# Optimization experiments

Measured on AMD Instinct MI355X. Metric: run time of the kernel, lower is better.

## Reference

```python
import math
import jax, jax.numpy as jnp
import numpy as np

B = 2
TMAX = 1024
D = 1024
H = 16
DK = D // H
F = 4096
L = 2
CHUNK = 128
LEFT = 128
RIGHT = 32
EPS = 1e-5


def _build_mask(t_max, chunk, left, right):
    """Replicates EmformerEncoder.create_mask with audio_lens == t_max.
    Returns bool [T, T] where True = masked (disallowed), T = total_right + t_max."""
    num_chunks = math.ceil(t_max / chunk)
    ub = (num_chunks - 1) * right
    body = np.zeros((t_max, t_max), np.float32)
    mleft = np.zeros((t_max, ub), np.float32)
    mdiag = np.zeros((ub, ub), np.float32)
    mright = np.zeros((ub, t_max), np.float32)
    right_indexes = []
    for i in range(num_chunks):
        left_off = max(chunk * i - left, 0)
        start = chunk * i
        end = min(chunk * (i + 1), t_max)
        body[start:end, left_off:end] = 1
        if i == num_chunks - 1:
            break
        rem = t_max - (end + right)
        trl = right if rem >= 0 else t_max - end
        ri = len(right_indexes)
        mleft[start:start + chunk, ri:ri + trl] = 1
        mdiag[ri:ri + trl, ri:ri + trl] = 1
        mright[ri:ri + trl, left_off:end] = 1
        right_indexes += list(range(end, end + trl))
    rs = len(right_indexes)
    mleft = mleft[:, :rs]
    mdiag = mdiag[:rs, :rs]
    mright = mright[:rs, :]
    top = np.concatenate([mdiag, mright], axis=-1)
    bot = np.concatenate([mleft, body], axis=-1)
    m = np.concatenate([top, bot], axis=0)
    return m == 0  # True where attention is NOT allowed


def setup_inputs() -> dict:
    key = jax.random.key(0)
    ks = jax.random.split(key, 8)
    mask2d = _build_mask(TMAX, CHUNK, LEFT, RIGHT)  # [T, T]
    T = mask2d.shape[0]  # 1248
    w = lambda k, shape: jax.random.normal(k, shape, jnp.float32) * 0.02
    inp = {
        "input": jax.random.normal(ks[0], (B, T, D), jnp.float32),
        "ln_in_scale": jnp.ones((L, D), jnp.float32),
        "ln_in_bias": jnp.zeros((L, D), jnp.float32),
        "Wq": w(ks[1], (L, D, D)), "bq": jnp.zeros((L, D), jnp.float32),
        "Wk": w(ks[2], (L, D, D)), "bk": jnp.zeros((L, D), jnp.float32),
        "Wv": w(ks[3], (L, D, D)), "bv": jnp.zeros((L, D), jnp.float32),
        "ln1_scale": jnp.ones((L, D), jnp.float32),
        "ln1_bias": jnp.zeros((L, D), jnp.float32),
        "W1": w(ks[4], (L, D, F)), "b1": jnp.zeros((L, F), jnp.float32),
        "W2": w(ks[5], (L, F, D)), "b2": jnp.zeros((L, D), jnp.float32),
        "ln2_scale": jnp.ones((L, D), jnp.float32),
        "ln2_bias": jnp.zeros((L, D), jnp.float32),
        "mask": jnp.asarray(np.broadcast_to(mask2d[None, None], (B, 1, T, T)).copy()),
    }
    return inp


def _ln(x, scale, bias):
    m = jnp.mean(x, axis=-1, keepdims=True)
    v = jnp.mean(jnp.square(x - m), axis=-1, keepdims=True)
    return (x - m) * jax.lax.rsqrt(v + EPS) * scale + bias


def reference(input, ln_in_scale, ln_in_bias, Wq, bq, Wk, bk, Wv, bv,
              ln1_scale, ln1_bias, W1, b1, W2, b2, ln2_scale, ln2_bias, mask):
    x = input
    Bx, T, _ = x.shape
    scale = 1.0 / math.sqrt(DK)
    for l in range(L):
        h = _ln(x, ln_in_scale[l], ln_in_bias[l])  # pre-LN input (also residual base)
        q = (h @ Wq[l] + bq[l]).reshape(Bx, T, H, DK)
        k = (h @ Wk[l] + bk[l]).reshape(Bx, T, H, DK)
        v = (h @ Wv[l] + bv[l]).reshape(Bx, T, H, DK)
        scores = jnp.einsum('bqhd,bkhd->bhqk', q, k) * scale  # [B,H,T,T]
        scores = jnp.where(mask, -jnp.inf, scores)
        probs = jax.nn.softmax(scores, axis=-1)
        probs = jnp.where(mask, 0.0, probs)  # dropout_attn=0 -> identity
        o = jnp.einsum('bhqk,bkhd->bqhd', probs, v).reshape(Bx, T, D)
        attn_out = o + h
        y = _ln(attn_out, ln1_scale[l], ln1_bias[l])
        y = y @ W1[l] + b1[l]          # note: no activation in original code
        y = y @ W2[l] + b2[l] + attn_out
        x = _ln(y, ln2_scale[l], ln2_bias[l])
    return x
```

## Files before the change

### kernel.cpp

```cpp
#include <hip/hip_runtime.h>
#include <stdint.h>

typedef __attribute__((ext_vector_type(8))) short short8;
typedef __attribute__((ext_vector_type(4))) float f32x4;
typedef __attribute__((ext_vector_type(2))) _Float16 half2_t;

#define DEV __device__ __forceinline__

DEV float bits2f(uint32_t u){ union{uint32_t u;float f;}v; v.u=u; return v.f; }
DEV float bf_lo(uint32_t w){ return bits2f(w<<16); }
DEV float bf_hi(uint32_t w){ return bits2f(w & 0xffff0000u); }
DEV float bf1(uint16_t s){ return bits2f(((uint32_t)s)<<16); }
DEV uint16_t f2bf(float f){ union{float f;uint32_t u;}v; v.f=f; uint32_t u=v.u;
  return (uint16_t)((u + 0x7fffu + ((u>>16)&1u))>>16); }
DEV uint32_t pk16(float a, float b){ union{_Float16 h[2]; uint32_t u;}v;
  v.h[0]=(_Float16)a; v.h[1]=(_Float16)b; return v.u; }
DEV uint16_t f2h(float a){ union{_Float16 h; uint16_t u;}v; v.h=(_Float16)a; return v.u; }
DEV float h2f(uint16_t s){ union{uint16_t u; _Float16 h;}v; v.u=s; return (float)v.h; }

DEV float ldval(const float* p, size_t i){ return p[i]; }
DEV float ldval(const uint16_t* p, size_t i){ return bf1(p[i]); }
DEV void stval(float* p, size_t i, float v){ p[i]=v; }
DEV void stval(uint16_t* p, size_t i, float v){ p[i]=f2bf(v); }

DEV void async16(const void* g, void* l){
#if __has_builtin(__builtin_amdgcn_global_load_lds)
  __builtin_amdgcn_global_load_lds((const __attribute__((address_space(1))) void*)g,
                                   (__attribute__((address_space(3))) void*)l, 16, 0, 0);
#else
  int lane = threadIdx.x & 63;
  *(uint4*)((char*)l + lane*16) = *(const uint4*)((const char*)g);
#endif
}

template<int TM, bool SPLIT>
__global__ __launch_bounds__(256) void gemm_t(
    const uint16_t* __restrict__ A, const uint16_t* __restrict__ Bt,
    const float* __restrict__ bias, void* __restrict__ Cout,
    int N, int K, int kchunk) {
  __shared__ uint16_t sA[TM*32];
  __shared__ uint16_t sB[128*32];
  const int m0 = blockIdx.y*TM, n0 = blockIdx.x*128;
  const int kb = SPLIT ? blockIdx.z*kchunk : 0;
  const int kend = SPLIT ? kb + kchunk : K;
  const int tid = threadIdx.x, wid = tid>>6, lane = tid&63;
  constexpr int WM = TM/2;
  constexpr int MT = WM/16;
  const int wm = (wid&1)*WM, wn = (wid>>1)*64;
  f32x4 acc[MT][4];
  #pragma unroll
  for (int a=0;a<MT;a++)
    #pragma unroll
    for (int b=0;b<4;b++) acc[a][b] = (f32x4){0.f,0.f,0.f,0.f};
  const int lrow = lane>>2, lcol = (lane&3)*8;

  for (int k0 = kb; k0 < kend; k0 += 32) {
    __syncthreads();
    #pragma unroll
    for (int j = 0; j < TM/64; ++j) {
      int r0 = wid*(TM/4) + j*16;
      async16(A + (size_t)(m0 + r0 + lrow)*K + k0 + lcol, &sA[r0*32]);
    }
    #pragma unroll
    for (int j = 0; j < 2; ++j) {
      int r0 = wid*32 + j*16;
      async16(Bt + (size_t)(n0 + r0 + lrow)*K + k0 + lcol, &sB[r0*32]);
    }
    __syncthreads();
    short8 af[MT], bfv[4];
    #pragma unroll
    for (int t=0;t<MT;t++) af[t] = *(const short8*)&sA[(wm + t*16 + (lane&15))*32 + (lane>>4)*8];
    #pragma unroll
    for (int t=0;t<4;t++)  bfv[t] = *(const short8*)&sB[(wn + t*16 + (lane&15))*32 + (lane>>4)*8];
    #pragma unroll
    for (int mt=0;mt<MT;mt++)
      #pragma unroll
      for (int nt=0;nt<4;nt++)
        acc[mt][nt] = __builtin_amdgcn_mfma_f32_16x16x32_bf16(af[mt], bfv[nt], acc[mt][nt], 0,0,0);
  }
  const int cl = lane&15, rl = (lane>>4)*4;
  if (SPLIT) {
    float* Pz = (float*)Cout + (size_t)blockIdx.z*2560*N;
    #pragma unroll
    for (int nt=0;nt<4;nt++) {
      int n = n0 + wn + nt*16 + cl;
      #pragma unroll
      for (int mt=0;mt<MT;mt++)
        #pragma unroll
        for (int r=0;r<4;r++)
          Pz[(size_t)(m0 + wm + mt*16 + rl + r)*N + n] = acc[mt][nt][r];
    }
  } else {
    uint16_t* C = (uint16_t*)Cout;
    #pragma unroll
    for (int nt=0;nt<4;nt++) {
      int n = n0 + wn + nt*16 + cl;
      float bv = bias ? bias[n] : 0.f;
      #pragma unroll
      for (int mt=0;mt<MT;mt++)
        #pragma unroll
        for (int r=0;r<4;r++)
          C[(size_t)(m0 + wm + mt*16 + rl + r)*N + n] = f2bf(acc[mt][nt][r] + bv);
    }
  }
}

template<typename TI, typename TO>
__global__ __launch_bounds__(256) void ln_k(const TI* __restrict__ x,
    const float* __restrict__ sc, const float* __restrict__ bi,
    TO* __restrict__ out) {
  const int row = blockIdx.x, tid = threadIdx.x;
  const size_t base = (size_t)row*1024 + tid*4;
  float v0=ldval(x,base), v1=ldval(x,base+1), v2=ldval(x,base+2), v3=ldval(x,base+3);
  float s = v0+v1+v2+v3;
  float sq = v0*v0+v1*v1+v2*v2+v3*v3;
  #pragma unroll
  for (int off=32; off; off>>=1){ s += __shfl_xor(s,off); sq += __shfl_xor(sq,off); }
  __shared__ float red[8];
  int wid=tid>>6, lane=tid&63;
  if (lane==0){ red[wid]=s; red[4+wid]=sq; }
  __syncthreads();
  s = red[0]+red[1]+red[2]+red[3]; sq = red[4]+red[5]+red[6]+red[7];
  float mean = s*(1.f/1024.f);
  float inv  = rsqrtf(sq*(1.f/1024.f) - mean*mean + 1e-5f);
  int c = tid*4;
  stval(out, base,   (v0-mean)*inv*sc[c]   + bi[c]);
  stval(out, base+1, (v1-mean)*inv*sc[c+1] + bi[c+1]);
  stval(out, base+2, (v2-mean)*inv*sc[c+2] + bi[c+2]);
  stval(out, base+3, (v3-mean)*inv*sc[c+3] + bi[c+3]);
}

template<typename TO>
__global__ __launch_bounds__(256) void ln2_fused(const float* __restrict__ P,
    const float* __restrict__ b2, const uint16_t* __restrict__ resid,
    const float* __restrict__ sc, const float* __restrict__ bi,
    TO* __restrict__ out) {
  const int row = blockIdx.x, tid = threadIdx.x;
  const size_t base = (size_t)row*1024 + tid*4;
  float4 p0 = *(const float4*)(P + base);
  float4 p1 = *(const float4*)(P + (size_t)2560*1024 + base);
  int c = tid*4;
  float v0 = p0.x+p1.x+b2[c]  +bf1(resid[base]);
  float v1 = p0.y+p1.y+b2[c+1]+bf1(resid[base+1]);
  float v2 = p0.z+p1.z+b2[c+2]+bf1(resid[base+2]);
  float v3 = p0.w+p1.w+b2[c+3]+bf1(resid[base+3]);
  float s = v0+v1+v2+v3;
  float sq = v0*v0+v1*v1+v2*v2+v3*v3;
  #pragma unroll
  for (int off=32; off; off>>=1){ s += __shfl_xor(s,off); sq += __shfl_xor(sq,off); }
  __shared__ float red[8];
  int wid=tid>>6, lane=tid&63;
  if (lane==0){ red[wid]=s; red[4+wid]=sq; }
  __syncthreads();
  s = red[0]+red[1]+red[2]+red[3]; sq = red[4]+red[5]+red[6]+red[7];
  float mean = s*(1.f/1024.f);
  float inv  = rsqrtf(sq*(1.f/1024.f) - mean*mean + 1e-5f);
  stval(out, base,   (v0-mean)*inv*sc[c]   + bi[c]);
  stval(out, base+1, (v1-mean)*inv*sc[c+1] + bi[c+1]);
  stval(out, base+2, (v2-mean)*inv*sc[c+2] + bi[c+2]);
  stval(out, base+3, (v3-mean)*inv*sc[c+3] + bi[c+3]);
}

__global__ __launch_bounds__(256) void attn_fused(
    const uint32_t* __restrict__ qkv32, const uint16_t* __restrict__ hres,
    uint16_t* __restrict__ attn_out) {
  const int blk = blockIdx.x;
  const int qg = blk & 3, ci = (blk>>2)&7, hh = (blk>>5)&15, bb = blk>>9;
  const int sum_cnt = (ci<7)?32:0;
  const int bstart = (ci>=1)?128*(ci-1):0;
  const int bend = (ci==7)?1024:128*(ci+1);
  const int nk = sum_cnt + (bend - bstart);
  const int rowbase = bb*1248;
  const int tid = threadIdx.x, wid = tid>>6, lane = tid&63;
  const int fr = lane&15, fc = lane>>4;

  __shared__ uint16_t sm[32576];
  uint16_t* K16 = sm;
  uint32_t* KD  = (uint32_t*)sm;
  uint16_t* Q16 = sm + 20736;
  uint32_t* QD  = (uint32_t*)(sm + 20736);
  uint16_t* S16 = sm;
  uint16_t* P16 = sm + 20736;
  uint16_t* VT16 = sm;

  for (int idx = tid; idx < nk*32; idx += 256) {
    int j = idx>>5, d2 = idx&31;
    int tk = (j < sum_cnt) ? (32*ci + j) : (224 + bstart + (j - sum_cnt));
    uint32_t u = qkv32[(size_t)(rowbase+tk)*1536 + 512 + hh*32 + d2];
    KD[j*36 + d2] = pk16(bf_lo(u), bf_hi(u));
  }
  for (int idx = tid; idx < 40*32; idx += 256) {
    int j = idx>>5, d2 = idx&31;
    int ql = qg*40 + j;
    int tq = (ql<32) ? (32*ci+ql) : (224+128*ci+ql-32);
    uint32_t u = qkv32[(size_t)(rowbase+tq)*1536 + hh*32 + d2];
    QD[j*36 + d2] = pk16(bf_lo(u), bf_hi(u));
  }
  __syncthreads();

  const int n_mt = nk>>4;
  const int qoff[3] = {0,16,24};
  f32x4 accs[5][3];
  #pragma unroll
  for (int a=0;a<5;a++)
    #pragma unroll
    for (int b=0;b<3;b++) accs[a][b] = (f32x4){0.f,0.f,0.f,0.f};
  #pragma unroll
  for (int ks=0; ks<2; ++ks) {
    short8 bq_[3];
    #pragma unroll
    for (int nt=0;nt<3;nt++)
      bq_[nt] = *(const short8*)&Q16[(qoff[nt]+fr)*72 + ks*32 + fc*8];
    #pragma unroll
    for (int t=0;t<5;t++) {
      int mt = wid + 4*t;
      if (mt < n_mt) {
        short8 a_ = *(const short8*)&K16[(mt*16+fr)*72 + ks*32 + fc*8];
        #pragma unroll
        for (int nt=0;nt<3;nt++)
          accs[t][nt] = __builtin_amdgcn_mfma_f32_16x16x32_f16(a_, bq_[nt], accs[t][nt], 0,0,0);
      }
    }
  }
  __syncthreads();

  #pragma unroll
  for (int t=0;t<5;t++) {
    int mt = wid + 4*t;
    if (mt < n_mt) {
      #pragma unroll
      for (int nt=0;nt<3;nt++) {
        int q = qoff[nt] + fr;
        #pragma unroll
        for (int r=0;r<4;r++)
          S16[q*296 + mt*16 + fc*4 + r] = f2h(accs[t][nt][r]*0.125f);
      }
    }
  }
  __syncthreads();

  for (int i=0;i<10;i++) {
    int row = wid*10 + i;
    float v[5];
    #pragma unroll
    for (int g=0;g<5;g++){ int k=g*64+lane; v[g] = (k<nk) ? h2f(S16[row*296+k]) : -1e30f; }
    float mx = fmaxf(fmaxf(fmaxf(v[0],v[1]),fmaxf(v[2],v[3])),v[4]);
    #pragma unroll
    for (int off=32; off; off>>=1) mx = fmaxf(mx, __shfl_xor(mx,off));
    float p[5], sum=0.f;
    #pragma unroll
    for (int g=0;g<5;g++){ p[g] = __expf(v[g]-mx); if (g*64+lane>=nk) p[g]=0.f; sum+=p[g]; }
    #pragma unroll
    for (int off=32; off; off>>=1) sum += __shfl_xor(sum,off);
    float inv = 1.f/sum;
    #pragma unroll
    for (int g=0;g<5;g++){ int k=g*64+lane; if (k<nk) P16[row*296+k] = f2h(p[g]*inv); }
  }
  __syncthreads();

  for (int idx = tid; idx < nk*32; idx += 256) {
    int j = idx>>5, d2 = idx&31;
    int tk = (j < sum_cnt) ? (32*ci + j) : (224 + bstart + (j - sum_cnt));
    uint32_t u = qkv32[(size_t)(rowbase+tk)*1536 + 1024 + hh*32 + d2];
    VT16[(2*d2)*296 + j]   = f2h(bf_lo(u));
    VT16[(2*d2+1)*296 + j] = f2h(bf_hi(u));
  }
  __syncthreads();

  const int nkt = nk>>5;
  f32x4 acco[3];
  #pragma unroll
  for (int t=0;t<3;t++) acco[t] = (f32x4){0.f,0.f,0.f,0.f};
  for (int kt=0; kt<nkt; ++kt) {
    short8 bv_ = *(const short8*)&VT16[(wid*16+fr)*296 + kt*32 + fc*8];
    #pragma unroll
    for (int t=0;t<3;t++) {
      short8 a_ = *(const short8*)&P16[(qoff[t]+fr)*296 + kt*32 + fc*8];
      acco[t] = __builtin_amdgcn_mfma_f32_16x16x32_f16(a_, bv_, acco[t], 0,0,0);
    }
  }
  #pragma unroll
  for (int t=0;t<3;t++) {
    #pragma unroll
    for (int r=0;r<4;r++) {
      int ql = qg*40 + qoff[t] + fc*4 + r;
      bool vq = (ci<7) || (ql >= qg*40+32) || (qg>0);
      if (ci==7 && qg==0 && (qoff[t]+fc*4+r)<32) vq = false; else vq = true;
      if (vq) {
        int qll = qg*40 + qoff[t] + fc*4 + r;
        int tq = (qll<32) ? (32*ci+qll) : (224+128*ci+qll-32);
        size_t addr = (size_t)(rowbase+tq)*1024 + hh*64 + wid*16 + fr;
        attn_out[addr] = f2bf(acco[t][r] + bf1(hres[addr]));
      }
      (void)ql;
    }
  }
}

__global__ void prep_k(const float* __restrict__ Wq, const float* __restrict__ Wk,
                       const float* __restrict__ Wv, const float* __restrict__ W1,
                       const float* __restrict__ W2, const float* __restrict__ bq,
                       const float* __restrict__ bk, const float* __restrict__ bv,
                       uint16_t* __restrict__ wt_qkv, uint16_t* __restrict__ wt_w1,
                       uint16_t* __restrict__ wt_w2, float* __restrict__ bqkv) {
  __shared__ float t[32][33];
  const int blk = blockIdx.x;
  const int tx = threadIdx.x, ty = threadIdx.y;
  if (blk >= 11264) {
    int i = (blk-11264)*256 + ty*32 + tx;
    bqkv[i] = (i<1024) ? bq[i] : ((i<2048) ? bk[i-1024] : bv[i-2048]);
    return;
  }
  const float* src; uint16_t* dst; int R, C, c0, r0;
  if (blk < 3072) {
    int w = blk>>10, tt = blk&1023;
    src = (w==0)?Wq:((w==1)?Wk:Wv); dst = wt_qkv + (size_t)w*1048576;
    R = 1024; C = 1024; c0 = (tt&31)*32; r0 = (tt>>5)*32;
  } else if (blk < 7168) {
    int tt = blk-3072;
    src = W1; dst = wt_w1; R = 1024; C = 4096;
    c0 = (tt&127)*32; r0 = (tt>>7)*32;
  } else {
    int tt = blk-7168;
    src = W2; dst = wt_w2; R = 4096; C = 1024;
    c0 = (tt&31)*32; r0 = (tt>>5)*32;
  }
  #pragma unroll
  for (int i=0;i<4;i++) t[ty+8*i][tx] = src[(size_t)(r0+ty+8*i)*C + c0+tx];
  __syncthreads();
  #pragma unroll
  for (int i=0;i<4;i++) dst[(size_t)(c0+ty+8*i)*R + r0+tx] = f2bf(t[tx][ty+8*i]);
}

extern "C" void kernel_launch(void* const* d_in, const int* in_sizes, int n_in,
                              void* d_out, int out_size, void* d_ws, size_t ws_size,
                              hipStream_t stream) {
  const float* input  = (const float*)d_in[0];
  const float* lnin_s = (const float*)d_in[1];
  const float* lnin_b = (const float*)d_in[2];
  const float* Wq = (const float*)d_in[3];
  const float* bq = (const float*)d_in[4];
  const float* Wk = (const float*)d_in[5];
  const float* bk = (const float*)d_in[6];
  const float* Wv = (const float*)d_in[7];
  const float* bv = (const float*)d_in[8];
  const float* ln1_s = (const float*)d_in[9];
  const float* ln1_b = (const float*)d_in[10];
  const float* W1 = (const float*)d_in[11];
  const float* b1 = (const float*)d_in[12];
  const float* W2 = (const float*)d_in[13];
  const float* b2 = (const float*)d_in[14];
  const float* ln2_s = (const float*)d_in[15];
  const float* ln2_b = (const float*)d_in[16];

  char* ws = (char*)d_ws;
  uint16_t* wt_qkv = (uint16_t*)(ws + 0);
  uint16_t* wt_w1  = (uint16_t*)(ws + 6291456);
  uint16_t* wt_w2  = (uint16_t*)(ws + 14680064);
  float*    bqkv   = (float*)   (ws + 23068672);
  uint16_t* hbuf   = (uint16_t*)(ws + 23080960);
  uint16_t* qkvb   = (uint16_t*)(ws + 28323840);
  uint16_t* attnb  = (uint16_t*)(ws + 44052480);
  uint16_t* zbuf   = (uint16_t*)(ws + 49295360);
  float*    pbuf   = (float*)   (ws + 54538240);
  uint16_t* y1b    = hbuf;
  uint16_t* x1b    = zbuf;

  const uint16_t* xcur_bf = x1b;
  for (int l=0; l<2; ++l) {
    prep_k<<<11276, dim3(32,8), 0, stream>>>(Wq+(size_t)l*1048576, Wk+(size_t)l*1048576,
        Wv+(size_t)l*1048576, W1+(size_t)l*4194304, W2+(size_t)l*4194304,
        bq+l*1024, bk+l*1024, bv+l*1024, wt_qkv, wt_w1, wt_w2, bqkv);

    if (l==0) ln_k<float,uint16_t>   <<<2496,256,0,stream>>>(input,   lnin_s+l*1024, lnin_b+l*1024, hbuf);
    else      ln_k<uint16_t,uint16_t><<<2496,256,0,stream>>>(xcur_bf, lnin_s+l*1024, lnin_b+l*1024, hbuf);
    gemm_t<64,false><<<dim3(24,40),256,0,stream>>>(hbuf, wt_qkv, bqkv, qkvb, 3072, 1024, 1024);
    attn_fused<<<1024,256,0,stream>>>((const uint32_t*)qkvb, hbuf, attnb);
    ln_k<uint16_t,uint16_t><<<2496,256,0,stream>>>(attnb, ln1_s+l*1024, ln1_b+l*1024, zbuf);
    gemm_t<64,false><<<dim3(32,40),256,0,stream>>>(zbuf, wt_w1, b1+l*4096, y1b, 4096, 1024, 1024);
    gemm_t<64,true><<<dim3(8,40,2),256,0,stream>>>(y1b, wt_w2, nullptr, pbuf, 1024, 4096, 2048);
    if (l==1) ln2_fused<float>   <<<2496,256,0,stream>>>(pbuf, b2+l*1024, attnb, ln2_s+l*1024, ln2_b+l*1024, (float*)d_out);
    else      ln2_fused<uint16_t><<<2496,256,0,stream>>>(pbuf, b2+l*1024, attnb, ln2_s+l*1024, ln2_b+l*1024, x1b);
  }
  (void)in_sizes; (void)n_in; (void)out_size; (void)ws_size;
}
```

Measured before the change: 532.9 us.

## Double GEMM k-step to 64, add TN template, fuse input LN into prep kernel

The GEMM now loads two 32-wide k slices per sync, which halves the barrier count per k-loop. It also gains a TN template parameter so the W2 split-K GEMM can use 64-wide N tiles with a doubled grid. The input LayerNorm is folded into the weight-prep kernel as extra blocks, which removes one launch per layer. A dead variable in the attention store is cleaned up. Shared memory per GEMM block grows, which may reduce occupancy.

```diff
diff --git a/kernel.cpp b/kernel.cpp
--- a/kernel.cpp
+++ b/kernel.cpp
@@ -33,56 +33,62 @@
 #endif
 }
 
-template<int TM, bool SPLIT>
+template<int TM, int TN, bool SPLIT>
 __global__ __launch_bounds__(256) void gemm_t(
     const uint16_t* __restrict__ A, const uint16_t* __restrict__ Bt,
     const float* __restrict__ bias, void* __restrict__ Cout,
     int N, int K, int kchunk) {
-  __shared__ uint16_t sA[TM*32];
-  __shared__ uint16_t sB[128*32];
-  const int m0 = blockIdx.y*TM, n0 = blockIdx.x*128;
+  __shared__ uint16_t sA[2][TM*32];
+  __shared__ uint16_t sB[2][TN*32];
+  const int m0 = blockIdx.y*TM, n0 = blockIdx.x*TN;
   const int kb = SPLIT ? blockIdx.z*kchunk : 0;
   const int kend = SPLIT ? kb + kchunk : K;
   const int tid = threadIdx.x, wid = tid>>6, lane = tid&63;
-  constexpr int WM = TM/2;
-  constexpr int MT = WM/16;
-  const int wm = (wid&1)*WM, wn = (wid>>1)*64;
-  f32x4 acc[MT][4];
+  constexpr int WM = TM/2, MT = WM/16;
+  constexpr int WN = TN/2, NT = WN/16;
+  const int wm = (wid&1)*WM, wn = (wid>>1)*WN;
+  f32x4 acc[MT][NT];
   #pragma unroll
   for (int a=0;a<MT;a++)
     #pragma unroll
-    for (int b=0;b<4;b++) acc[a][b] = (f32x4){0.f,0.f,0.f,0.f};
+    for (int b=0;b<NT;b++) acc[a][b] = (f32x4){0.f,0.f,0.f,0.f};
   const int lrow = lane>>2, lcol = (lane&3)*8;
 
-  for (int k0 = kb; k0 < kend; k0 += 32) {
+  for (int k0 = kb; k0 < kend; k0 += 64) {
     __syncthreads();
     #pragma unroll
-    for (int j = 0; j < TM/64; ++j) {
-      int r0 = wid*(TM/4) + j*16;
-      async16(A + (size_t)(m0 + r0 + lrow)*K + k0 + lcol, &sA[r0*32]);
-    }
-    #pragma unroll
-    for (int j = 0; j < 2; ++j) {
-      int r0 = wid*32 + j*16;
-      async16(Bt + (size_t)(n0 + r0 + lrow)*K + k0 + lcol, &sB[r0*32]);
+    for (int h=0; h<2; ++h) {
+      #pragma unroll
+      for (int j = 0; j < TM/64; ++j) {
+        int r0 = wid*(TM/4) + j*16;
+        async16(A + (size_t)(m0+r0+lrow)*K + k0+h*32 + lcol, &sA[h][r0*32]);
+      }
+      #pragma unroll
+      for (int j = 0; j < TN/64; ++j) {
+        int r0 = wid*(TN/4) + j*16;
+        async16(Bt + (size_t)(n0+r0+lrow)*K + k0+h*32 + lcol, &sB[h][r0*32]);
+      }
     }
     __syncthreads();
-    short8 af[MT], bfv[4];
-    #pragma unroll
-    for (int t=0;t<MT;t++) af[t] = *(const short8*)&sA[(wm + t*16 + (lane&15))*32 + (lane>>4)*8];
-    #pragma unroll
-    for (int t=0;t<4;t++)  bfv[t] = *(const short8*)&sB[(wn + t*16 + (lane&15))*32 + (lane>>4)*8];
-    #pragma unroll
-    for (int mt=0;mt<MT;mt++)
-      #pragma unroll
-      for (int nt=0;nt<4;nt++)
-        acc[mt][nt] = __builtin_amdgcn_mfma_f32_16x16x32_bf16(af[mt], bfv[nt], acc[mt][nt], 0,0,0);
+    #pragma unroll
+    for (int h=0; h<2; ++h) {
+      short8 af[MT], bfv[NT];
+      #pragma unroll
+      for (int t=0;t<MT;t++) af[t] = *(const short8*)&sA[h][(wm + t*16 + (lane&15))*32 + (lane>>4)*8];
+      #pragma unroll
+      for (int t=0;t<NT;t++) bfv[t] = *(const short8*)&sB[h][(wn + t*16 + (lane&15))*32 + (lane>>4)*8];
+      #pragma unroll
+      for (int mt=0;mt<MT;mt++)
+        #pragma unroll
+        for (int nt=0;nt<NT;nt++)
+          acc[mt][nt] = __builtin_amdgcn_mfma_f32_16x16x32_bf16(af[mt], bfv[nt], acc[mt][nt], 0,0,0);
+    }
   }
   const int cl = lane&15, rl = (lane>>4)*4;
   if (SPLIT) {
     float* Pz = (float*)Cout + (size_t)blockIdx.z*2560*N;
     #pragma unroll
-    for (int nt=0;nt<4;nt++) {
+    for (int nt=0;nt<NT;nt++) {
       int n = n0 + wn + nt*16 + cl;
       #pragma unroll
       for (int mt=0;mt<MT;mt++)
@@ -93,7 +99,7 @@
   } else {
     uint16_t* C = (uint16_t*)Cout;
     #pragma unroll
-    for (int nt=0;nt<4;nt++) {
+    for (int nt=0;nt<NT;nt++) {
       int n = n0 + wn + nt*16 + cl;
       float bv = bias ? bias[n] : 0.f;
       #pragma unroll
@@ -106,17 +112,14 @@
 }
 
 template<typename TI, typename TO>
-__global__ __launch_bounds__(256) void ln_k(const TI* __restrict__ x,
-    const float* __restrict__ sc, const float* __restrict__ bi,
-    TO* __restrict__ out) {
-  const int row = blockIdx.x, tid = threadIdx.x;
+DEV void ln_body(int row, int tid, const TI* x, const float* sc, const float* bi,
+                 TO* out, float* red) {
   const size_t base = (size_t)row*1024 + tid*4;
   float v0=ldval(x,base), v1=ldval(x,base+1), v2=ldval(x,base+2), v3=ldval(x,base+3);
   float s = v0+v1+v2+v3;
   float sq = v0*v0+v1*v1+v2*v2+v3*v3;
   #pragma unroll
   for (int off=32; off; off>>=1){ s += __shfl_xor(s,off); sq += __shfl_xor(sq,off); }
-  __shared__ float red[8];
   int wid=tid>>6, lane=tid&63;
   if (lane==0){ red[wid]=s; red[4+wid]=sq; }
   __syncthreads();
@@ -128,6 +131,14 @@
   stval(out, base+1, (v1-mean)*inv*sc[c+1] + bi[c+1]);
   stval(out, base+2, (v2-mean)*inv*sc[c+2] + bi[c+2]);
   stval(out, base+3, (v3-mean)*inv*sc[c+3] + bi[c+3]);
+}
+
+template<typename TI, typename TO>
+__global__ __launch_bounds__(256) void ln_k(const TI* __restrict__ x,
+    const float* __restrict__ sc, const float* __restrict__ bi,
+    TO* __restrict__ out) {
+  __shared__ float red[8];
+  ln_body<TI,TO>(blockIdx.x, threadIdx.x, x, sc, bi, out, red);
 }
 
 template<typename TO>
@@ -283,16 +294,14 @@
   for (int t=0;t<3;t++) {
     #pragma unroll
     for (int r=0;r<4;r++) {
-      int ql = qg*40 + qoff[t] + fc*4 + r;
-      bool vq = (ci<7) || (ql >= qg*40+32) || (qg>0);
-      if (ci==7 && qg==0 && (qoff[t]+fc*4+r)<32) vq = false; else vq = true;
+      bool vq = true;
+      if (ci==7 && qg==0 && (qoff[t]+fc*4+r)<32) vq = false;
       if (vq) {
         int qll = qg*40 + qoff[t] + fc*4 + r;
         int tq = (qll<32) ? (32*ci+qll) : (224+128*ci+qll-32);
         size_t addr = (size_t)(rowbase+tq)*1024 + hh*64 + wid*16 + fr;
         attn_out[addr] = f2bf(acco[t][r] + bf1(hres[addr]));
       }
-      (void)ql;
     }
   }
 }
@@ -302,10 +311,21 @@
                        const float* __restrict__ W2, const float* __restrict__ bq,
                        const float* __restrict__ bk, const float* __restrict__ bv,
                        uint16_t* __restrict__ wt_qkv, uint16_t* __restrict__ wt_w1,
-                       uint16_t* __restrict__ wt_w2, float* __restrict__ bqkv) {
+                       uint16_t* __restrict__ wt_w2, float* __restrict__ bqkv,
+                       const void* __restrict__ lnx, int lnx_f32,
+                       const float* __restrict__ lnsc, const float* __restrict__ lnbi,
+                       uint16_t* __restrict__ lnout) {
   __shared__ float t[32][33];
   const int blk = blockIdx.x;
   const int tx = threadIdx.x, ty = threadIdx.y;
+  if (blk >= 11276) {
+    int row = blk - 11276;
+    int tid = ty*32 + tx;
+    float* red = &t[0][0];
+    if (lnx_f32) ln_body<float,uint16_t>((int)row, tid, (const float*)lnx, lnsc, lnbi, lnout, red);
+    else         ln_body<uint16_t,uint16_t>((int)row, tid, (const uint16_t*)lnx, lnsc, lnbi, lnout, red);
+    return;
+  }
   if (blk >= 11264) {
     int i = (blk-11264)*256 + ty*32 + tx;
     bqkv[i] = (i<1024) ? bq[i] : ((i<2048) ? bk[i-1024] : bv[i-2048]);
@@ -368,17 +388,17 @@
 
   const uint16_t* xcur_bf = x1b;
   for (int l=0; l<2; ++l) {
-    prep_k<<<11276, dim3(32,8), 0, stream>>>(Wq+(size_t)l*1048576, Wk+(size_t)l*1048576,
+    prep_k<<<13772, dim3(32,8), 0, stream>>>(Wq+(size_t)l*1048576, Wk+(size_t)l*1048576,
         Wv+(size_t)l*1048576, W1+(size_t)l*4194304, W2+(size_t)l*4194304,
-        bq+l*1024, bk+l*1024, bv+l*1024, wt_qkv, wt_w1, wt_w2, bqkv);
-
-    if (l==0) ln_k<float,uint16_t>   <<<2496,256,0,stream>>>(input,   lnin_s+l*1024, lnin_b+l*1024, hbuf);
-    else      ln_k<uint16_t,uint16_t><<<2496,256,0,stream>>>(xcur_bf, lnin_s+l*1024, lnin_b+l*1024, hbuf);
-    gemm_t<64,false><<<dim3(24,40),256,0,stream>>>(hbuf, wt_qkv, bqkv, qkvb, 3072, 1024, 1024);
+        bq+l*1024, bk+l*1024, bv+l*1024, wt_qkv, wt_w1, wt_w2, bqkv,
+        (l==0) ? (const void*)input : (const void*)xcur_bf, (l==0)?1:0,
+        lnin_s+l*1024, lnin_b+l*1024, hbuf);
+
+    gemm_t<64,128,false><<<dim3(24,40),256,0,stream>>>(hbuf, wt_qkv, bqkv, qkvb, 3072, 1024, 1024);
     attn_fused<<<1024,256,0,stream>>>((const uint32_t*)qkvb, hbuf, attnb);
     ln_k<uint16_t,uint16_t><<<2496,256,0,stream>>>(attnb, ln1_s+l*1024, ln1_b+l*1024, zbuf);
-    gemm_t<64,false><<<dim3(32,40),256,0,stream>>>(zbuf, wt_w1, b1+l*4096, y1b, 4096, 1024, 1024);
-    gemm_t<64,true><<<dim3(8,40,2),256,0,stream>>>(y1b, wt_w2, nullptr, pbuf, 1024, 4096, 2048);
+    gemm_t<64,128,false><<<dim3(32,40),256,0,stream>>>(zbuf, wt_w1, b1+l*4096, y1b, 4096, 1024, 1024);
+    gemm_t<64,64,true><<<dim3(16,40,2),256,0,stream>>>(y1b, wt_w2, nullptr, pbuf, 1024, 4096, 2048);
     if (l==1) ln2_fused<float>   <<<2496,256,0,stream>>>(pbuf, b2+l*1024, attnb, ln2_s+l*1024, ln2_b+l*1024, (float*)d_out);
     else      ln2_fused<uint16_t><<<2496,256,0,stream>>>(pbuf, b2+l*1024, attnb, ln2_s+l*1024, ln2_b+l*1024, x1b);
   }
```

New measurement: 507.8 us. 1.05x faster.
